# Performance work log

Hardware: AMD Instinct MI355X
Metric: run time of the kernel (lower is better)

The kernel has to match this reference:

```python
import jax, jax.numpy as jnp
import numpy as np

B = 256      # graph pairs
NPG = 28     # nodes per graph
MAXN = 32    # max_node_set_size
EPG = 64     # edges per graph (== max_edge_set_size, so no edge padding)
MAXE = 64
D = 128      # node_state_dim
FN = 32      # raw node feature dim
FE = 32      # raw edge feature dim
SK = 64      # sinkhorn_feature_dim
STEPS = 3    # propagation_steps
TEMP = 0.1
ITERS = 20
CW = 0.9     # consistency_weight
G = 2 * B
N = G * NPG
E = G * EPG


def _lin(key, fi, fo):
    return jax.random.normal(key, (fi, fo), jnp.float32) / np.sqrt(fi)


def setup_inputs() -> dict:
    key = jax.random.key(0)
    ks = jax.random.split(key, 12)
    rng = np.random.default_rng(0)
    off = (np.arange(G) * NPG)[:, None]   # graphs ordered q0,c0,q1,c1,...
    from_idx = jnp.asarray((rng.integers(0, NPG, (G, EPG)) + off).reshape(-1), jnp.int32)
    to_idx = jnp.asarray((rng.integers(0, NPG, (G, EPG)) + off).reshape(-1), jnp.int32)
    return dict(
        node_features=jax.random.normal(ks[0], (N, FN), jnp.float32),
        edge_features=jax.random.normal(ks[1], (E, FE), jnp.float32),
        enc_nw=_lin(ks[2], FN, D), enc_nb=jnp.zeros((D,), jnp.float32),
        enc_ew=_lin(ks[3], FE, D), enc_eb=jnp.zeros((D,), jnp.float32),
        msg_w1=_lin(ks[4], 3 * D, 2 * D), msg_b1=jnp.zeros((2 * D,), jnp.float32),
        msg_w2=_lin(ks[5], 2 * D, D), msg_b2=jnp.zeros((D,), jnp.float32),
        rmsg_w1=_lin(ks[6], 3 * D, 2 * D), rmsg_b1=jnp.zeros((2 * D,), jnp.float32),
        rmsg_w2=_lin(ks[7], 2 * D, D), rmsg_b2=jnp.zeros((D,), jnp.float32),
        upd_w1=_lin(ks[8], 2 * D, 2 * D), upd_b1=jnp.zeros((2 * D,), jnp.float32),
        upd_w2=_lin(ks[9], 2 * D, D), upd_b2=jnp.zeros((D,), jnp.float32),
        sk_w1=_lin(ks[10], D, SK), sk_b1=jnp.zeros((SK,), jnp.float32),
        sk_w2=_lin(ks[11], SK, SK), sk_b2=jnp.zeros((SK,), jnp.float32),
        from_idx=from_idx, to_idx=to_idx,
        query_sizes=jnp.full((B,), NPG, jnp.int32),
        corpus_sizes=jnp.full((B,), NPG, jnp.int32),
    )


def _mlp2(x, w1, b1, w2, b2):
    return jnp.maximum(x @ w1 + b1, 0.0) @ w2 + b2


def _sinkhorn(log_alpha):
    # log-domain sinkhorn (noise_factor = 0 -> deterministic)
    la = log_alpha / TEMP
    for _ in range(ITERS):
        la = la - jax.nn.logsumexp(la, axis=2, keepdims=True)
        la = la - jax.nn.logsumexp(la, axis=1, keepdims=True)
    return jnp.exp(la)


def _align(q, c, plan):
    # feature_alignment_score: -relu(q - P @ c).sum over set and feature dims
    return -jnp.maximum(q - plan @ c, 0.0).sum(axis=(1, 2))


def _forward(node_features, edge_features, enc_nw, enc_nb, enc_ew, enc_eb,
             msg_w1, msg_b1, msg_w2, msg_b2, rmsg_w1, rmsg_b1, rmsg_w2, rmsg_b2,
             upd_w1, upd_b1, upd_w2, upd_b2, sk_w1, sk_b1, sk_w2, sk_b2,
             from_idx, to_idx, query_sizes, corpus_sizes):
    h = node_features @ enc_nw + enc_nb        # encoder, [N, D]
    e = edge_features @ enc_ew + enc_eb        # [E, D]

    def messages(h):
        f = _mlp2(jnp.concatenate([h[from_idx], h[to_idx], e], -1), msg_w1, msg_b1, msg_w2, msg_b2)
        r = _mlp2(jnp.concatenate([h[to_idx], h[from_idx], e], -1), rmsg_w1, rmsg_b1, rmsg_w2, rmsg_b2)
        return f, r

    for _ in range(STEPS):  # GraphPropLayer x propagation_steps
        f, r = messages(h)
        agg = jax.ops.segment_sum(f, to_idx, num_segments=N) + \
              jax.ops.segment_sum(r, from_idx, num_segments=N)
        h = h + _mlp2(jnp.concatenate([agg, h], -1), upd_w1, upd_b1, upd_w2, upd_b2)

    # split_and_stack nodes: graphs alternate query/corpus, pad NPG -> MAXN
    hs = jnp.pad(h.reshape(B, 2, NPG, D), ((0, 0), (0, 0), (0, MAXN - NPG), (0, 0)))
    q_nodes, c_nodes = hs[:, 0], hs[:, 1]      # [B, MAXN, D]

    tq = _mlp2(q_nodes, sk_w1, sk_b1, sk_w2, sk_b2)
    tc = _mlp2(c_nodes, sk_w1, sk_b1, sk_w2, sk_b2)
    pos = jnp.arange(MAXN)[None, :]
    mq = tq * (pos < query_sizes[:, None])[..., None]
    mc = tc * (pos < corpus_sizes[:, None])[..., None]
    node_plan = _sinkhorn(jnp.einsum('bqd,bcd->bqc', mq, mc))   # [B, MAXN, MAXN]

    # propagation_messages on final node states
    f, r = messages(h)
    em = (f + r).reshape(B, 2, EPG, D)         # EPG == MAXE -> no pad
    q_edges, c_edges = em[:, 0], em[:, 1]

    # local (within-graph) endpoint indices for kronecker lookup
    fl = (from_idx % NPG).reshape(B, 2, EPG)
    tl = (to_idx % NPG).reshape(B, 2, EPG)
    qf, cf = fl[:, 0], fl[:, 1]
    qt, ct = tl[:, 0], tl[:, 1]

    def kron(T, qf, qt, cf, ct):
        straight = T[qf][:, cf] * T[qt][:, ct]   # [MAXE, MAXE]
        cross = T[qf][:, ct] * T[qt][:, cf]
        return straight + cross

    edge_scores = jax.vmap(kron)(node_plan, qf, qt, cf, ct)     # [B, MAXE, MAXE]
    edge_plan = _sinkhorn(edge_scores)

    return _align(q_nodes, c_nodes, node_plan) + CW * _align(q_edges, c_edges, edge_plan)


def reference(node_features, edge_features, enc_nw, enc_nb, enc_ew, enc_eb,
              msg_w1, msg_b1, msg_w2, msg_b2, rmsg_w1, rmsg_b1, rmsg_w2, rmsg_b2,
              upd_w1, upd_b1, upd_w2, upd_b2, sk_w1, sk_b1, sk_w2, sk_b2,
              from_idx, to_idx, query_sizes, corpus_sizes):
    return _forward(node_features, edge_features, enc_nw, enc_nb, enc_ew, enc_eb,
                    msg_w1, msg_b1, msg_w2, msg_b2, rmsg_w1, rmsg_b1, rmsg_w2, rmsg_b2,
                    upd_w1, upd_b1, upd_w2, upd_b2, sk_w1, sk_b1, sk_w2, sk_b2,
                    from_idx, to_idx, query_sizes, corpus_sizes)
```

## Files before the change

kernel.cpp:

```cpp
#include <hip/hip_runtime.h>
#include <math.h>

#define NPG 28
#define EPG 64
#define NB  256
#define NG  512
#define NN  14336
#define NE  32768
#define TEMPINV 10.0f
#define SINK_ITERS 20
#define CW 0.9f

typedef unsigned int uint;
typedef unsigned short ushort;
typedef __attribute__((ext_vector_type(8))) __bf16 bf16x8;
typedef __attribute__((ext_vector_type(4))) float f32x4;

__device__ __forceinline__ ushort f2bf(float x) {
    uint u = __float_as_uint(x);
    u += 0x7fffu + ((u >> 16) & 1u);
    return (ushort)(u >> 16);
}
__device__ __forceinline__ uint f2bf2(float lo, float hi) {
    return (uint)f2bf(lo) | ((uint)f2bf(hi) << 16);
}
__device__ __forceinline__ float bflo(uint w) { return __uint_as_float(w << 16); }
__device__ __forceinline__ float bfhi(uint w) { return __uint_as_float(w & 0xffff0000u); }
__device__ __forceinline__ uint relu_sum_pk(uint w1, uint w2, uint w3) {
    float lo = fmaxf(bflo(w1) + bflo(w2) + bflo(w3), 0.f);
    float hi = fmaxf(bfhi(w1) + bfhi(w2) + bfhi(w3), 0.f);
    return f2bf2(lo, hi);
}
__device__ __forceinline__ f32x4 mfma16(bf16x8 a, bf16x8 b, f32x4 c) {
    return __builtin_amdgcn_mfma_f32_16x16x32_bf16(a, b, c, 0, 0, 0);
}

__global__ __launch_bounds__(512, 4) void gnn_fused(
    float* __restrict__ h,
    const ushort* __restrict__ EC2,
    const ushort* __restrict__ WhpL,
    const ushort* __restrict__ W2fL, const ushort* __restrict__ W2rL,
    const float* __restrict__ b2f, const float* __restrict__ b2r,
    const ushort* __restrict__ UW1T, const float* __restrict__ ub1,
    const ushort* __restrict__ UW2T, const float* __restrict__ ub2,
    const int* __restrict__ from_idx, const int* __restrict__ to_idx,
    float* __restrict__ EM)
{
    __shared__ ushort HPs[NPG * 520];
    __shared__ float acc_s[NPG * 132];
    __shared__ float hs[NPG * 132];
    __shared__ int fl[64], tl[64];
    const int g = blockIdx.x;
    const int tid = threadIdx.x;
    const int w = tid >> 6, lane = tid & 63;
    const int li = lane & 15, quad = lane >> 4;
    const int wm = w >> 1, wn = w & 1;
    ushort* hid = &HPs[0];

    if (tid < 64) {
        fl[tid] = from_idx[g * 64 + tid] - g * NPG;
        tl[tid] = to_idx[g * 64 + tid] - g * NPG;
    }
    for (int u = tid; u < NPG * 128; u += 512)
        hs[(u >> 7) * 132 + (u & 127)] = h[(size_t)g * (NPG * 128) + u];
    __syncthreads();

#pragma unroll 1
    for (int step = 0; step < 3; ++step) {
        uint4 ha[2][4];
#pragma unroll
        for (int mi = 0; mi < 2; ++mi) {
            const int row = mi * 16 + li;
            const int rr = (row < NPG) ? row : 0;
#pragma unroll
            for (int kb = 0; kb < 4; ++kb) {
                const float* src = &hs[rr * 132 + kb * 32 + quad * 8];
                const float4 f0 = *(const float4*)src;
                const float4 f1 = *(const float4*)(src + 4);
                uint4 o;
                o.x = f2bf2(f0.x, f0.y);
                o.y = f2bf2(f0.z, f0.w);
                o.z = f2bf2(f1.x, f1.y);
                o.w = f2bf2(f1.z, f1.w);
                ha[mi][kb] = o;
            }
        }
        for (int u = tid; u < NPG * 132; u += 512) acc_s[u] = 0.f;

        f32x4 acc[4];
#pragma unroll
        for (int j = 0; j < 4; ++j) acc[j] = f32x4{0.f, 0.f, 0.f, 0.f};

#pragma unroll 1
        for (int p = 0; p < 2; ++p) {
            {
                const int colw = w * 64;
#pragma unroll
                for (int ni = 0; ni < 4; ++ni) {
                    const int col = colw + ni * 16 + li;
                    const ushort* pb = WhpL + (size_t)(p * 512 + col) * 32 + quad * 8;
                    f32x4 c0 = f32x4{0.f, 0.f, 0.f, 0.f};
                    f32x4 c1 = f32x4{0.f, 0.f, 0.f, 0.f};
#pragma unroll
                    for (int kb = 0; kb < 4; ++kb) {
                        const bf16x8 b = __builtin_bit_cast(bf16x8,
                            *(const uint4*)(pb + (size_t)kb * 32768));
                        c0 = mfma16(__builtin_bit_cast(bf16x8, ha[0][kb]), b, c0);
                        c1 = mfma16(__builtin_bit_cast(bf16x8, ha[1][kb]), b, c1);
                    }
#pragma unroll
                    for (int r = 0; r < 4; ++r) {
                        const int r0 = quad * 4 + r;
                        HPs[r0 * 520 + col] = f2bf(c0[r]);
                        const int r1 = 16 + quad * 4 + r;
                        if (r1 < NPG) HPs[r1 * 520 + col] = f2bf(c1[r]);
                    }
                }
            }
            __syncthreads();
            if (p == 1) {
#pragma unroll
                for (int j = 0; j < 4; ++j) acc[j] = f32x4{0.f, 0.f, 0.f, 0.f};
            }
            const int e = wm * 16 + li;
            const int i1 = p ? tl[e] : fl[e];
            const int i2 = p ? fl[e] : tl[e];
            const int ad1 = i1 * 520 + quad * 8;
            const int ad2 = i2 * 520 + 256 + quad * 8;
            const int ade = e * 32 + quad * 8;
            const ushort* ecb = EC2 + (size_t)(g * 2 + p) * 16384;
            const ushort* W2L = p ? W2rL : W2fL;
            const int n0 = wn * 64;
            const ushort* pb[4];
#pragma unroll
            for (int ni = 0; ni < 4; ++ni)
                pb[ni] = W2L + (size_t)(n0 + ni * 16 + li) * 32 + quad * 8;
#pragma unroll
            for (int kb = 0; kb < 8; ++kb) {
                const uint4 u1 = *(const uint4*)&HPs[ad1 + kb * 32];
                const uint4 u2 = *(const uint4*)&HPs[ad2 + kb * 32];
                const uint4 ue = *(const uint4*)(ecb + kb * 2048 + ade);
                uint4 o;
                o.x = relu_sum_pk(u1.x, u2.x, ue.x);
                o.y = relu_sum_pk(u1.y, u2.y, ue.y);
                o.z = relu_sum_pk(u1.z, u2.z, ue.z);
                o.w = relu_sum_pk(u1.w, u2.w, ue.w);
                const bf16x8 a = __builtin_bit_cast(bf16x8, o);
#pragma unroll
                for (int ni = 0; ni < 4; ++ni) {
                    const bf16x8 b = __builtin_bit_cast(bf16x8,
                        *(const uint4*)(pb[ni] + (size_t)kb * 4096));
                    acc[ni] = mfma16(a, b, acc[ni]);
                }
            }
            {
                const int* targ = p ? fl : tl;
                const float* bias = p ? b2r : b2f;
                float bv[4];
#pragma unroll
                for (int ni = 0; ni < 4; ++ni) bv[ni] = bias[n0 + ni * 16 + li];
#pragma unroll
                for (int r = 0; r < 4; ++r) {
                    const int loc = targ[wm * 16 + quad * 4 + r];
#pragma unroll
                    for (int ni = 0; ni < 4; ++ni)
                        atomicAdd(&acc_s[loc * 132 + n0 + ni * 16 + li],
                                  acc[ni][r] + bv[ni]);
                }
            }
            __syncthreads();
        }

        {
            const int n0u = w * 32;
            f32x4 ua[2][2];
#pragma unroll
            for (int mi = 0; mi < 2; ++mi)
#pragma unroll
                for (int ni = 0; ni < 2; ++ni) ua[mi][ni] = f32x4{0.f, 0.f, 0.f, 0.f};
            const ushort* pb0 = UW1T + (size_t)(n0u + li) * 256 + quad * 8;
            const ushort* pb1 = UW1T + (size_t)(n0u + 16 + li) * 256 + quad * 8;
#pragma unroll
            for (int kb = 0; kb < 8; ++kb) {
                bf16x8 a[2];
                if (kb < 4) {
#pragma unroll
                    for (int mi = 0; mi < 2; ++mi) {
                        const int row = mi * 16 + li;
                        const int rr = (row < NPG) ? row : 0;
                        const float* src = &acc_s[rr * 132 + kb * 32 + quad * 8];
                        const float4 f0 = *(const float4*)src;
                        const float4 f1 = *(const float4*)(src + 4);
                        uint4 o;
                        o.x = f2bf2(f0.x, f0.y);
                        o.y = f2bf2(f0.z, f0.w);
                        o.z = f2bf2(f1.x, f1.y);
                        o.w = f2bf2(f1.z, f1.w);
                        a[mi] = __builtin_bit_cast(bf16x8, o);
                    }
                } else {
                    a[0] = __builtin_bit_cast(bf16x8, ha[0][kb - 4]);
                    a[1] = __builtin_bit_cast(bf16x8, ha[1][kb - 4]);
                }
                const bf16x8 b0 = __builtin_bit_cast(bf16x8, *(const uint4*)(pb0 + kb * 32));
                const bf16x8 b1 = __builtin_bit_cast(bf16x8, *(const uint4*)(pb1 + kb * 32));
#pragma unroll
                for (int mi = 0; mi < 2; ++mi) {
                    ua[mi][0] = mfma16(a[mi], b0, ua[mi][0]);
                    ua[mi][1] = mfma16(a[mi], b1, ua[mi][1]);
                }
            }
            const float bv0 = ub1[n0u + li], bv1 = ub1[n0u + 16 + li];
#pragma unroll
            for (int mi = 0; mi < 2; ++mi)
#pragma unroll
                for (int r = 0; r < 4; ++r) {
                    const int row = mi * 16 + quad * 4 + r;
                    if (row < NPG) {
                        hid[row * 264 + n0u + li] = f2bf(fmaxf(ua[mi][0][r] + bv0, 0.f));
                        hid[row * 264 + n0u + 16 + li] = f2bf(fmaxf(ua[mi][1][r] + bv1, 0.f));
                    }
                }
        }
        __syncthreads();
        {
            const int n0u = w * 16;
            f32x4 ua[2];
            ua[0] = f32x4{0.f, 0.f, 0.f, 0.f};
            ua[1] = f32x4{0.f, 0.f, 0.f, 0.f};
            const ushort* pb0 = UW2T + (size_t)(n0u + li) * 256 + quad * 8;
#pragma unroll
            for (int kb = 0; kb < 8; ++kb) {
                bf16x8 a[2];
#pragma unroll
                for (int mi = 0; mi < 2; ++mi) {
                    const int row = mi * 16 + li;
                    const int rr = (row < NPG) ? row : 0;
                    a[mi] = __builtin_bit_cast(bf16x8,
                        *(const uint4*)&hid[rr * 264 + kb * 32 + quad * 8]);
                }
                const bf16x8 b0 = __builtin_bit_cast(bf16x8, *(const uint4*)(pb0 + kb * 32));
                ua[0] = mfma16(a[0], b0, ua[0]);
                ua[1] = mfma16(a[1], b0, ua[1]);
            }
            const float bv = ub2[n0u + li];
#pragma unroll
            for (int mi = 0; mi < 2; ++mi)
#pragma unroll
                for (int r = 0; r < 4; ++r) {
                    const int row = mi * 16 + quad * 4 + r;
                    if (row < NPG)
                        hs[row * 132 + n0u + li] += ua[mi][r] + bv;
                }
        }
        __syncthreads();
    }

    {
        uint4 ha[2][4];
#pragma unroll
        for (int mi = 0; mi < 2; ++mi) {
            const int row = mi * 16 + li;
            const int rr = (row < NPG) ? row : 0;
#pragma unroll
            for (int kb = 0; kb < 4; ++kb) {
                const float* src = &hs[rr * 132 + kb * 32 + quad * 8];
                const float4 f0 = *(const float4*)src;
                const float4 f1 = *(const float4*)(src + 4);
                uint4 o;
                o.x = f2bf2(f0.x, f0.y);
                o.y = f2bf2(f0.z, f0.w);
                o.z = f2bf2(f1.x, f1.y);
                o.w = f2bf2(f1.z, f1.w);
                ha[mi][kb] = o;
            }
        }
        f32x4 acc[4];
#pragma unroll
        for (int j = 0; j < 4; ++j) acc[j] = f32x4{0.f, 0.f, 0.f, 0.f};
        const int n0 = wn * 64;
#pragma unroll 1
        for (int p = 0; p < 2; ++p) {
            {
                const int colw = w * 64;
#pragma unroll
                for (int ni = 0; ni < 4; ++ni) {
                    const int col = colw + ni * 16 + li;
                    const ushort* pb = WhpL + (size_t)(p * 512 + col) * 32 + quad * 8;
                    f32x4 c0 = f32x4{0.f, 0.f, 0.f, 0.f};
                    f32x4 c1 = f32x4{0.f, 0.f, 0.f, 0.f};
#pragma unroll
                    for (int kb = 0; kb < 4; ++kb) {
                        const bf16x8 b = __builtin_bit_cast(bf16x8,
                            *(const uint4*)(pb + (size_t)kb * 32768));
                        c0 = mfma16(__builtin_bit_cast(bf16x8, ha[0][kb]), b, c0);
                        c1 = mfma16(__builtin_bit_cast(bf16x8, ha[1][kb]), b, c1);
                    }
#pragma unroll
                    for (int r = 0; r < 4; ++r) {
                        const int r0 = quad * 4 + r;
                        HPs[r0 * 520 + col] = f2bf(c0[r]);
                        const int r1 = 16 + quad * 4 + r;
                        if (r1 < NPG) HPs[r1 * 520 + col] = f2bf(c1[r]);
                    }
                }
            }
            __syncthreads();
            const int e = wm * 16 + li;
            const int i1 = p ? tl[e] : fl[e];
            const int i2 = p ? fl[e] : tl[e];
            const int ad1 = i1 * 520 + quad * 8;
            const int ad2 = i2 * 520 + 256 + quad * 8;
            const int ade = e * 32 + quad * 8;
            const ushort* ecb = EC2 + (size_t)(g * 2 + p) * 16384;
            const ushort* W2L = p ? W2rL : W2fL;
            const ushort* pb[4];
#pragma unroll
            for (int ni = 0; ni < 4; ++ni)
                pb[ni] = W2L + (size_t)(n0 + ni * 16 + li) * 32 + quad * 8;
#pragma unroll
            for (int kb = 0; kb < 8; ++kb) {
                const uint4 u1 = *(const uint4*)&HPs[ad1 + kb * 32];
                const uint4 u2 = *(const uint4*)&HPs[ad2 + kb * 32];
                const uint4 ue = *(const uint4*)(ecb + kb * 2048 + ade);
                uint4 o;
                o.x = relu_sum_pk(u1.x, u2.x, ue.x);
                o.y = relu_sum_pk(u1.y, u2.y, ue.y);
                o.z = relu_sum_pk(u1.z, u2.z, ue.z);
                o.w = relu_sum_pk(u1.w, u2.w, ue.w);
                const bf16x8 a = __builtin_bit_cast(bf16x8, o);
#pragma unroll
                for (int ni = 0; ni < 4; ++ni) {
                    const bf16x8 b = __builtin_bit_cast(bf16x8,
                        *(const uint4*)(pb[ni] + (size_t)kb * 4096));
                    acc[ni] = mfma16(a, b, acc[ni]);
                }
            }
            __syncthreads();
        }
        float bv[4];
#pragma unroll
        for (int ni = 0; ni < 4; ++ni)
            bv[ni] = b2f[n0 + ni * 16 + li] + b2r[n0 + ni * 16 + li];
#pragma unroll
        for (int r = 0; r < 4; ++r) {
            const int erow = g * 64 + wm * 16 + quad * 4 + r;
#pragma unroll
            for (int ni = 0; ni < 4; ++ni)
                EM[(size_t)erow * 128 + n0 + ni * 16 + li] = acc[ni][r] + bv[ni];
        }
    }
    for (int u = tid; u < NPG * 128; u += 512)
        h[(size_t)g * (NPG * 128) + u] = hs[(u >> 7) * 132 + (u & 127)];
}

template<int TM, bool OUTBF, bool OUT2, bool ECL>
__global__ __launch_bounds__(256) void gemm2(
    const float* __restrict__ A, int lda, int K,
    const float* __restrict__ W, int ldw, const float* __restrict__ bias,
    float* __restrict__ C, ushort* __restrict__ Cb, int ldc)
{
    constexpr int BM = TM * 16;
    constexpr int AV = BM / 64;
    __shared__ float As[16][BM + 4];
    __shared__ float Bs[16][132];
    const int tid = threadIdx.x;
    const int m0 = blockIdx.x * BM;
    const int n0 = blockIdx.y * 128;
    const int tx = tid & 15, ty = tid >> 4;
    const int arow = (AV == 2) ? (tid >> 1) : (tid >> 2);
    const int a0   = (AV == 2) ? ((tid & 1) * 8) : ((tid & 3) * 4);
    const int brow = ty;
    const int bcol = tx * 8;
    const int nch = K >> 4;

    float4 aC[2], bC[2], aN[2], bN[2];
    float acc[TM][8];
#pragma unroll
    for (int i = 0; i < TM; ++i)
#pragma unroll
        for (int j = 0; j < 8; ++j) acc[i][j] = 0.f;

    {
        const float* src = A + (size_t)(m0 + arow) * lda + a0;
        aC[0] = *(const float4*)src;
        if (AV == 2) aC[1] = *(const float4*)(src + 4);
        const float* bsrc = W + (size_t)brow * ldw + n0 + bcol;
        bC[0] = *(const float4*)bsrc;
        bC[1] = *(const float4*)(bsrc + 4);
    }

    for (int ch = 0; ch < nch; ++ch) {
        {
            const float* f = (const float*)aC;
#pragma unroll
            for (int i = 0; i < AV * 4; ++i) As[a0 + i][arow] = f[i];
            *(float4*)&Bs[brow][bcol]     = bC[0];
            *(float4*)&Bs[brow][bcol + 4] = bC[1];
        }
        __syncthreads();
        if (ch + 1 < nch) {
            const int kc = (ch + 1) << 4;
            const float* src = A + (size_t)(m0 + arow) * lda + kc + a0;
            aN[0] = *(const float4*)src;
            if (AV == 2) aN[1] = *(const float4*)(src + 4);
            const float* bsrc = W + (size_t)(kc + brow) * ldw + n0 + bcol;
            bN[0] = *(const float4*)bsrc;
            bN[1] = *(const float4*)(bsrc + 4);
        }
#pragma unroll
        for (int kk = 0; kk < 16; ++kk) {
            float afr[TM], bfr[8];
#pragma unroll
            for (int i = 0; i < TM; i += 4)
                *(float4*)&afr[i] = *(const float4*)&As[kk][ty * TM + i];
            *(float4*)&bfr[0] = *(const float4*)&Bs[kk][tx * 8];
            *(float4*)&bfr[4] = *(const float4*)&Bs[kk][tx * 8 + 4];
#pragma unroll
            for (int i = 0; i < TM; ++i)
#pragma unroll
                for (int j = 0; j < 8; ++j) acc[i][j] = fmaf(afr[i], bfr[j], acc[i][j]);
        }
        __syncthreads();
        aC[0] = aN[0]; aC[1] = aN[1];
        bC[0] = bN[0]; bC[1] = bN[1];
    }
#pragma unroll
    for (int i = 0; i < TM; ++i) {
        const int row = m0 + ty * TM + i;
#pragma unroll
        for (int j = 0; j < 8; ++j) {
            const int col = n0 + tx * 8 + j;
            float v = acc[i][j] + bias[col];
            if (ECL) {
                const int gg = row >> 6, eloc = row & 63;
                const int p = col >> 8, kb = (col >> 5) & 7, jj = col & 31;
                Cb[(size_t)(((gg * 2 + p) * 8 + kb)) * 2048 + eloc * 32 + jj] = f2bf(v);
            } else if (OUTBF) {
                Cb[(size_t)row * ldc + col] = f2bf(v);
            } else {
                C[(size_t)row * ldc + col] = v;
                if (OUT2) Cb[(size_t)row * ldc + col] = f2bf(v);
            }
        }
    }
}

__global__ __launch_bounds__(256) void pack2(
    const float* __restrict__ msg_w1, const float* __restrict__ rmsg_w1,
    const float* __restrict__ msg_b1, const float* __restrict__ rmsg_b1,
    const float* __restrict__ enc_ew, const float* __restrict__ enc_eb,
    const float* __restrict__ msg_w2, const float* __restrict__ rmsg_w2,
    const float* __restrict__ upd_w1, const float* __restrict__ upd_w2,
    float* __restrict__ Wcomb, float* __restrict__ bcomb,
    ushort* __restrict__ WhpL, ushort* __restrict__ W2fL, ushort* __restrict__ W2rL,
    ushort* __restrict__ UW1T, ushort* __restrict__ UW2T)
{
    const int gid = blockIdx.x, tid = threadIdx.x;
    if (gid < 64) {
        const int idx = gid * 256 + tid;
        const int a = idx >> 9, n = idx & 511;
        const float* Wsrc = (n < 256) ? msg_w1 : rmsg_w1;
        const int nc = n & 255;
        float s = 0.f;
        for (int j = 0; j < 128; ++j)
            s = fmaf(enc_ew[a * 128 + j], Wsrc[(256 + j) * 256 + nc], s);
        Wcomb[idx] = s;
    } else if (gid < 66) {
        const int n = (gid - 64) * 256 + tid;
        const float* Wsrc = (n < 256) ? msg_w1 : rmsg_w1;
        const float* bsrc = (n < 256) ? msg_b1 : rmsg_b1;
        const int nc = n & 255;
        float s = bsrc[nc];
        for (int j = 0; j < 128; ++j)
            s = fmaf(enc_eb[j], Wsrc[(256 + j) * 256 + nc], s);
        bcomb[n] = s;
    } else if (gid < 578) {
        const int idx = (gid - 66) * 256 + tid;
        const int n = idx >> 7, k = idx & 127;
        const float* Wsrc = (n < 512) ? msg_w1 : rmsg_w1;
        const int part = (n >> 8) & 1, col = n & 255;
        WhpL[(size_t)(k >> 5) * 32768 + n * 32 + (k & 31)] =
            f2bf(Wsrc[(part * 128 + k) * 256 + col]);
    } else if (gid < 706) {
        const int idx = (gid - 578) * 256 + tid;
        const int n = idx >> 8, k = idx & 255;
        W2fL[(size_t)(k >> 5) * 4096 + n * 32 + (k & 31)] = f2bf(msg_w2[k * 128 + n]);
    } else if (gid < 834) {
        const int idx = (gid - 706) * 256 + tid;
        const int n = idx >> 8, k = idx & 255;
        W2rL[(size_t)(k >> 5) * 4096 + n * 32 + (k & 31)] = f2bf(rmsg_w2[k * 128 + n]);
    } else if (gid < 1090) {
        const int idx = (gid - 834) * 256 + tid;
        const int n = idx >> 8, k = idx & 255;
        UW1T[idx] = f2bf(upd_w1[k * 256 + n]);
    } else {
        const int idx = (gid - 1090) * 256 + tid;
        const int n = idx >> 8, k = idx & 255;
        UW2T[idx] = f2bf(upd_w2[k * 128 + n]);
    }
}

__global__ __launch_bounds__(256) void node_kernel(
    const float* __restrict__ h,
    const float* __restrict__ w1, const float* __restrict__ b1,
    const float* __restrict__ w2, const float* __restrict__ b2,
    const int* __restrict__ qsz, const int* __restrict__ csz,
    float* __restrict__ plan_out, float* __restrict__ loss_out)
{
    __shared__ float qn[32][128];
    __shared__ float cn[32][128];
    __shared__ float t1[32][64];
    __shared__ float mq[32][68];
    __shared__ float mc[32][68];
    __shared__ float la[32][33];
    __shared__ float red[4];
    const int bb = blockIdx.x;
    const int tid = threadIdx.x;
    const int qs = qsz[bb], cs = csz[bb];
    for (int u = tid * 4; u < 4096; u += 1024) {
        const int p = u >> 7, d = u & 127;
        float4 zq = make_float4(0.f, 0.f, 0.f, 0.f), zc = zq;
        if (p < NPG) {
            zq = *(const float4*)(h + (size_t)((2 * bb) * NPG + p) * 128 + d);
            zc = *(const float4*)(h + (size_t)((2 * bb + 1) * NPG + p) * 128 + d);
        }
        *(float4*)&qn[p][d] = zq;
        *(float4*)&cn[p][d] = zc;
    }
    __syncthreads();
    const int col = tid & 63;
    const int rg  = tid >> 6;
    for (int s = 0; s < 2; ++s) {
        const float (*src)[128] = s ? cn : qn;
        float (*dst)[68] = s ? mc : mq;
        const int sz = s ? cs : qs;
        float a8[8];
#pragma unroll
        for (int u = 0; u < 8; ++u) a8[u] = b1[col];
        for (int k = 0; k < 128; ++k) {
            const float wv = w1[k * 64 + col];
#pragma unroll
            for (int u = 0; u < 8; ++u) a8[u] = fmaf(src[rg + 4 * u][k], wv, a8[u]);
        }
#pragma unroll
        for (int u = 0; u < 8; ++u) t1[rg + 4 * u][col] = fmaxf(a8[u], 0.f);
        __syncthreads();
#pragma unroll
        for (int u = 0; u < 8; ++u) a8[u] = b2[col];
        for (int k = 0; k < 64; ++k) {
            const float wv = w2[k * 64 + col];
#pragma unroll
            for (int u = 0; u < 8; ++u) a8[u] = fmaf(t1[rg + 4 * u][k], wv, a8[u]);
        }
#pragma unroll
        for (int u = 0; u < 8; ++u) {
            const int r = rg + 4 * u;
            dst[r][col] = (r < sz) ? a8[u] : 0.f;
        }
        __syncthreads();
    }
    {
        const int q = tid >> 3, cg = tid & 7;
#pragma unroll
        for (int u = 0; u < 4; ++u) {
            const int c = cg + 8 * u;
            float s = 0.f;
            for (int d = 0; d < 64; ++d) s = fmaf(mq[q][d], mc[c][d], s);
            la[q][c] = s * TEMPINV;
        }
    }
    __syncthreads();
    const int l8 = tid & 7, rq = tid >> 3;
    for (int it = 0; it < SINK_ITERS; ++it) {
        {
            float x[4];
#pragma unroll
            for (int u = 0; u < 4; ++u) x[u] = la[rq][l8 * 4 + u];
            float m = fmaxf(fmaxf(x[0], x[1]), fmaxf(x[2], x[3]));
            m = fmaxf(m, __shfl_xor(m, 1));
            m = fmaxf(m, __shfl_xor(m, 2));
            m = fmaxf(m, __shfl_xor(m, 4));
            float s = __expf(x[0] - m) + __expf(x[1] - m) + __expf(x[2] - m) + __expf(x[3] - m);
            s += __shfl_xor(s, 1);
            s += __shfl_xor(s, 2);
            s += __shfl_xor(s, 4);
            const float lse = m + __logf(s);
#pragma unroll
            for (int u = 0; u < 4; ++u) la[rq][l8 * 4 + u] = x[u] - lse;
        }
        __syncthreads();
        {
            float x[4];
#pragma unroll
            for (int u = 0; u < 4; ++u) x[u] = la[l8 * 4 + u][rq];
            float m = fmaxf(fmaxf(x[0], x[1]), fmaxf(x[2], x[3]));
            m = fmaxf(m, __shfl_xor(m, 1));
            m = fmaxf(m, __shfl_xor(m, 2));
            m = fmaxf(m, __shfl_xor(m, 4));
            float s = __expf(x[0] - m) + __expf(x[1] - m) + __expf(x[2] - m) + __expf(x[3] - m);
            s += __shfl_xor(s, 1);
            s += __shfl_xor(s, 2);
            s += __shfl_xor(s, 4);
            const float lse = m + __logf(s);
#pragma unroll
            for (int u = 0; u < 4; ++u) la[l8 * 4 + u][rq] = x[u] - lse;
        }
        __syncthreads();
    }
    for (int u = tid; u < 1024; u += 256) {
        const int q = u >> 5, c = u & 31;
        const float p = __expf(la[q][c]);
        la[q][c] = p;
        plan_out[(size_t)bb * 1024 + u] = p;
    }
    __syncthreads();
    float lsum = 0.f;
    {
        const int q = tid >> 3, dg = tid & 7;
        for (int u = 0; u < 16; ++u) {
            const int d = dg + 8 * u;
            float pc = 0.f;
#pragma unroll
            for (int c = 0; c < 32; ++c) pc = fmaf(la[q][c], cn[c][d], pc);
            lsum += fmaxf(qn[q][d] - pc, 0.f);
        }
    }
#pragma unroll
    for (int off = 1; off < 64; off <<= 1) lsum += __shfl_xor(lsum, off);
    if ((tid & 63) == 0) red[tid >> 6] = lsum;
    __syncthreads();
    if (tid == 0) loss_out[bb] = -(red[0] + red[1] + red[2] + red[3]);
}

__global__ __launch_bounds__(256) void edge_kernel(
    const float* __restrict__ plan, const float* __restrict__ EM,
    const int* __restrict__ from_idx, const int* __restrict__ to_idx,
    float* __restrict__ loss_out)
{
    __shared__ float T[32][33];
    __shared__ float la[64][65];
    __shared__ float ce[64][128];
    __shared__ int qf[64], qt[64], cfi[64], cti[64];
    __shared__ float red[4];
    const int bb = blockIdx.x;
    const int tid = threadIdx.x;
    for (int u = tid; u < 1024; u += 256) T[u >> 5][u & 31] = plan[(size_t)bb * 1024 + u];
    if (tid < 64) {
        const int gq = 2 * bb, gc = 2 * bb + 1;
        qf[tid]  = from_idx[gq * 64 + tid] - gq * NPG;
        qt[tid]  = to_idx  [gq * 64 + tid] - gq * NPG;
        cfi[tid] = from_idx[gc * 64 + tid] - gc * NPG;
        cti[tid] = to_idx  [gc * 64 + tid] - gc * NPG;
    }
    {
        const int gc = 2 * bb + 1;
        for (int u = tid * 4; u < 8192; u += 1024) {
            const int i = u >> 7, d = u & 127;
            *(float4*)&ce[i][d] = *(const float4*)(EM + (size_t)(gc * 64 + i) * 128 + d);
        }
    }
    __syncthreads();
    {
        const int i = tid >> 2, jg = tid & 3;
        const int a = qf[i], b_ = qt[i];
#pragma unroll
        for (int u = 0; u < 16; ++u) {
            const int j = jg * 16 + u;
            const float s = T[a][cfi[j]] * T[b_][cti[j]] + T[a][cti[j]] * T[b_][cfi[j]];
            la[i][j] = s * TEMPINV;
        }
    }
    __syncthreads();
    const int l4 = tid & 3, rr = tid >> 2;
    for (int it = 0; it < SINK_ITERS; ++it) {
        {
            float x[16];
#pragma unroll
            for (int u = 0; u < 16; ++u) x[u] = la[rr][l4 * 16 + u];
            float m = x[0];
#pragma unroll
            for (int u = 1; u < 16; ++u) m = fmaxf(m, x[u]);
            m = fmaxf(m, __shfl_xor(m, 1));
            m = fmaxf(m, __shfl_xor(m, 2));
            float s = 0.f;
#pragma unroll
            for (int u = 0; u < 16; ++u) s += __expf(x[u] - m);
            s += __shfl_xor(s, 1);
            s += __shfl_xor(s, 2);
            const float lse = m + __logf(s);
#pragma unroll
            for (int u = 0; u < 16; ++u) la[rr][l4 * 16 + u] = x[u] - lse;
        }
        __syncthreads();
        {
            float x[16];
#pragma unroll
            for (int u = 0; u < 16; ++u) x[u] = la[l4 * 16 + u][rr];
            float m = x[0];
#pragma unroll
            for (int u = 1; u < 16; ++u) m = fmaxf(m, x[u]);
            m = fmaxf(m, __shfl_xor(m, 1));
            m = fmaxf(m, __shfl_xor(m, 2));
            float s = 0.f;
#pragma unroll
            for (int u = 0; u < 16; ++u) s += __expf(x[u] - m);
            s += __shfl_xor(s, 1);
            s += __shfl_xor(s, 2);
            const float lse = m + __logf(s);
#pragma unroll
            for (int u = 0; u < 16; ++u) la[l4 * 16 + u][rr] = x[u] - lse;
        }
        __syncthreads();
    }
    for (int u = tid; u < 4096; u += 256) la[u >> 6][u & 63] = __expf(la[u >> 6][u & 63]);
    __syncthreads();
    float lsum = 0.f;
    {
        const int q = tid >> 2, dg = tid & 3;
        const float* qe = EM + (size_t)((2 * bb) * 64 + q) * 128;
        for (int u = 0; u < 32; ++u) {
            const int d = dg + 4 * u;
            float pc = 0.f;
            for (int c = 0; c < 64; ++c) pc = fmaf(la[q][c], ce[c][d], pc);
            lsum += fmaxf(qe[d] - pc, 0.f);
        }
    }
#pragma unroll
    for (int off = 1; off < 64; off <<= 1) lsum += __shfl_xor(lsum, off);
    if ((tid & 63) == 0) red[tid >> 6] = lsum;
    __syncthreads();
    if (tid == 0) loss_out[bb] -= CW * (red[0] + red[1] + red[2] + red[3]);
}

extern "C" void kernel_launch(void* const* d_in, const int* in_sizes, int n_in,
                              void* d_out, int out_size, void* d_ws, size_t ws_size,
                              hipStream_t stream)
{
    const float* node_features = (const float*)d_in[0];
    const float* edge_features = (const float*)d_in[1];
    const float* enc_nw  = (const float*)d_in[2];
    const float* enc_nb  = (const float*)d_in[3];
    const float* enc_ew  = (const float*)d_in[4];
    const float* enc_eb  = (const float*)d_in[5];
    const float* msg_w1  = (const float*)d_in[6];
    const float* msg_b1  = (const float*)d_in[7];
    const float* msg_w2  = (const float*)d_in[8];
    const float* msg_b2  = (const float*)d_in[9];
    const float* rmsg_w1 = (const float*)d_in[10];
    const float* rmsg_b1 = (const float*)d_in[11];
    const float* rmsg_w2 = (const float*)d_in[12];
    const float* rmsg_b2 = (const float*)d_in[13];
    const float* upd_w1  = (const float*)d_in[14];
    const float* upd_b1  = (const float*)d_in[15];
    const float* upd_w2  = (const float*)d_in[16];
    const float* upd_b2  = (const float*)d_in[17];
    const float* sk_w1   = (const float*)d_in[18];
    const float* sk_b1   = (const float*)d_in[19];
    const float* sk_w2   = (const float*)d_in[20];
    const float* sk_b2   = (const float*)d_in[21];
    const int* from_idx  = (const int*)d_in[22];
    const int* to_idx    = (const int*)d_in[23];
    const int* qsizes    = (const int*)d_in[24];
    const int* csizes    = (const int*)d_in[25];
    float* out = (float*)d_out;

    float* ws    = (float*)d_ws;
    float* h     = ws;
    float* EM    = h + (size_t)NN * 128;
    float* plan  = EM + (size_t)NE * 128;
    float* Wcomb = plan + (size_t)NB * 1024;
    float* bcomb = Wcomb + 16384;
    ushort* EC2  = (ushort*)(bcomb + 512);
    ushort* WhpL = EC2 + (size_t)NE * 512;
    ushort* W2fL = WhpL + 131072;
    ushort* W2rL = W2fL + 32768;
    ushort* UW1T = W2rL + 32768;
    ushort* UW2T = UW1T + 65536;

    const dim3 blk(256);
    const dim3 blk512(512);

    pack2<<<1218, blk, 0, stream>>>(msg_w1, rmsg_w1, msg_b1, rmsg_b1,
                                    enc_ew, enc_eb, msg_w2, rmsg_w2, upd_w1, upd_w2,
                                    Wcomb, bcomb, WhpL, W2fL, W2rL, UW1T, UW2T);
    gemm2<4, false, false, false><<<dim3(NN / 64, 1), blk, 0, stream>>>(
        node_features, 32, 32, enc_nw, 128, enc_nb, h, nullptr, 128);
    gemm2<8, false, false, true><<<dim3(NE / 128, 4), blk, 0, stream>>>(
        edge_features, 32, 32, Wcomb, 512, bcomb, nullptr, EC2, 512);

    gnn_fused<<<dim3(NG), blk512, 0, stream>>>(
        h, EC2, WhpL, W2fL, W2rL, msg_b2, rmsg_b2,
        UW1T, upd_b1, UW2T, upd_b2, from_idx, to_idx, EM);

    node_kernel<<<NB, blk, 0, stream>>>(
        h, sk_w1, sk_b1, sk_w2, sk_b2, qsizes, csizes, plan, out);
    edge_kernel<<<NB, blk, 0, stream>>>(
        plan, EM, from_idx, to_idx, out);
}
```

Measured before the change: 553.7 us.

## Fuse node and edge encoder GEMMs into gnn_fused with LDS-resident edge contributions

Removes the two separate fp32 encoder GEMM launches and computes the node encoding and the combined edge-encoder/message-W1 projection inside gnn_fused with bf16 MFMA. The per-graph edge contribution is stored in a new 64 KB LDS buffer instead of a global EC2 array, so it is no longer written to and re-read from global memory. Weights are pre-packed to bf16 in pack2. The cost is much higher LDS use per block, and the launch-bounds occupancy hint is dropped. The node encoder now runs in bf16 rather than fp32.

```diff
diff --git a/kernel.cpp b/kernel.cpp
--- a/kernel.cpp
+++ b/kernel.cpp
@@ -31,22 +31,34 @@
     float hi = fmaxf(bfhi(w1) + bfhi(w2) + bfhi(w3), 0.f);
     return f2bf2(lo, hi);
 }
+__device__ __forceinline__ uint4 pack_f32x8(const float* src) {
+    const float4 f0 = *(const float4*)src;
+    const float4 f1 = *(const float4*)(src + 4);
+    uint4 o;
+    o.x = f2bf2(f0.x, f0.y);
+    o.y = f2bf2(f0.z, f0.w);
+    o.z = f2bf2(f1.x, f1.y);
+    o.w = f2bf2(f1.z, f1.w);
+    return o;
+}
 __device__ __forceinline__ f32x4 mfma16(bf16x8 a, bf16x8 b, f32x4 c) {
     return __builtin_amdgcn_mfma_f32_16x16x32_bf16(a, b, c, 0, 0, 0);
 }
 
-__global__ __launch_bounds__(512, 4) void gnn_fused(
-    float* __restrict__ h,
-    const ushort* __restrict__ EC2,
+__global__ __launch_bounds__(512) void gnn_fused(
+    const float* __restrict__ nf, const float* __restrict__ ef,
+    const ushort* __restrict__ encL, const float* __restrict__ enc_nb,
+    const ushort* __restrict__ WcombL, const float* __restrict__ bcomb,
     const ushort* __restrict__ WhpL,
     const ushort* __restrict__ W2fL, const ushort* __restrict__ W2rL,
     const float* __restrict__ b2f, const float* __restrict__ b2r,
     const ushort* __restrict__ UW1T, const float* __restrict__ ub1,
     const ushort* __restrict__ UW2T, const float* __restrict__ ub2,
     const int* __restrict__ from_idx, const int* __restrict__ to_idx,
-    float* __restrict__ EM)
+    float* __restrict__ h, float* __restrict__ EM)
 {
     __shared__ ushort HPs[NPG * 520];
+    __shared__ ushort ECs[2 * 8 * 2048];
     __shared__ float acc_s[NPG * 132];
     __shared__ float hs[NPG * 132];
     __shared__ int fl[64], tl[64];
@@ -61,8 +73,65 @@
         fl[tid] = from_idx[g * 64 + tid] - g * NPG;
         tl[tid] = to_idx[g * 64 + tid] - g * NPG;
     }
-    for (int u = tid; u < NPG * 128; u += 512)
-        hs[(u >> 7) * 132 + (u & 127)] = h[(size_t)g * (NPG * 128) + u];
+
+    {
+        uint4 anf[2];
+#pragma unroll
+        for (int mi = 0; mi < 2; ++mi) {
+            const int row = mi * 16 + li;
+            const int rr = (row < NPG) ? row : 0;
+            const float4 f0 = *(const float4*)(nf + ((size_t)g * NPG + rr) * 32 + quad * 8);
+            const float4 f1 = *(const float4*)(nf + ((size_t)g * NPG + rr) * 32 + quad * 8 + 4);
+            uint4 o;
+            o.x = f2bf2(f0.x, f0.y); o.y = f2bf2(f0.z, f0.w);
+            o.z = f2bf2(f1.x, f1.y); o.w = f2bf2(f1.z, f1.w);
+            anf[mi] = o;
+        }
+        const int col = w * 16 + li;
+        const bf16x8 b = __builtin_bit_cast(bf16x8,
+            *(const uint4*)(encL + (size_t)col * 32 + quad * 8));
+        f32x4 c0 = mfma16(__builtin_bit_cast(bf16x8, anf[0]), b, f32x4{0.f, 0.f, 0.f, 0.f});
+        f32x4 c1 = mfma16(__builtin_bit_cast(bf16x8, anf[1]), b, f32x4{0.f, 0.f, 0.f, 0.f});
+        const float bv = enc_nb[col];
+#pragma unroll
+        for (int r = 0; r < 4; ++r) {
+            const int r0 = quad * 4 + r;
+            hs[r0 * 132 + col] = c0[r] + bv;
+            const int r1 = 16 + quad * 4 + r;
+            if (r1 < NPG) hs[r1 * 132 + col] = c1[r] + bv;
+        }
+    }
+    {
+        uint4 aef[4];
+#pragma unroll
+        for (int mi = 0; mi < 4; ++mi) {
+            const int e = mi * 16 + li;
+            const float4 f0 = *(const float4*)(ef + ((size_t)g * 64 + e) * 32 + quad * 8);
+            const float4 f1 = *(const float4*)(ef + ((size_t)g * 64 + e) * 32 + quad * 8 + 4);
+            uint4 o;
+            o.x = f2bf2(f0.x, f0.y); o.y = f2bf2(f0.z, f0.w);
+            o.z = f2bf2(f1.x, f1.y); o.w = f2bf2(f1.z, f1.w);
+            aef[mi] = o;
+        }
+#pragma unroll
+        for (int ni = 0; ni < 4; ++ni) {
+            const int col = w * 64 + ni * 16 + li;
+            const bf16x8 b = __builtin_bit_cast(bf16x8,
+                *(const uint4*)(WcombL + (size_t)col * 32 + quad * 8));
+            const float bv = bcomb[col];
+            const int pp = col >> 8, kbl = (col >> 5) & 7, j = col & 31;
+#pragma unroll
+            for (int mi = 0; mi < 4; ++mi) {
+                f32x4 c = mfma16(__builtin_bit_cast(bf16x8, aef[mi]), b,
+                                 f32x4{0.f, 0.f, 0.f, 0.f});
+#pragma unroll
+                for (int r = 0; r < 4; ++r) {
+                    const int e = mi * 16 + quad * 4 + r;
+                    ECs[pp * 16384 + kbl * 2048 + e * 32 + j] = f2bf(c[r] + bv);
+                }
+            }
+        }
+    }
     __syncthreads();
 
 #pragma unroll 1
@@ -73,17 +142,8 @@
             const int row = mi * 16 + li;
             const int rr = (row < NPG) ? row : 0;
 #pragma unroll
-            for (int kb = 0; kb < 4; ++kb) {
-                const float* src = &hs[rr * 132 + kb * 32 + quad * 8];
-                const float4 f0 = *(const float4*)src;
-                const float4 f1 = *(const float4*)(src + 4);
-                uint4 o;
-                o.x = f2bf2(f0.x, f0.y);
-                o.y = f2bf2(f0.z, f0.w);
-                o.z = f2bf2(f1.x, f1.y);
-                o.w = f2bf2(f1.z, f1.w);
-                ha[mi][kb] = o;
-            }
+            for (int kb = 0; kb < 4; ++kb)
+                ha[mi][kb] = pack_f32x8(&hs[rr * 132 + kb * 32 + quad * 8]);
         }
         for (int u = tid; u < NPG * 132; u += 512) acc_s[u] = 0.f;
 
@@ -118,6 +178,7 @@
                 }
             }
             __syncthreads();
+
             if (p == 1) {
 #pragma unroll
                 for (int j = 0; j < 4; ++j) acc[j] = f32x4{0.f, 0.f, 0.f, 0.f};
@@ -127,8 +188,7 @@
             const int i2 = p ? fl[e] : tl[e];
             const int ad1 = i1 * 520 + quad * 8;
             const int ad2 = i2 * 520 + 256 + quad * 8;
-            const int ade = e * 32 + quad * 8;
-            const ushort* ecb = EC2 + (size_t)(g * 2 + p) * 16384;
+            const int ade = p * 16384 + e * 32 + quad * 8;
             const ushort* W2L = p ? W2rL : W2fL;
             const int n0 = wn * 64;
             const ushort* pb[4];
@@ -139,7 +199,7 @@
             for (int kb = 0; kb < 8; ++kb) {
                 const uint4 u1 = *(const uint4*)&HPs[ad1 + kb * 32];
                 const uint4 u2 = *(const uint4*)&HPs[ad2 + kb * 32];
-                const uint4 ue = *(const uint4*)(ecb + kb * 2048 + ade);
+                const uint4 ue = *(const uint4*)&ECs[ade + kb * 2048];
                 uint4 o;
                 o.x = relu_sum_pk(u1.x, u2.x, ue.x);
                 o.y = relu_sum_pk(u1.y, u2.y, ue.y);
@@ -188,15 +248,8 @@
                     for (int mi = 0; mi < 2; ++mi) {
                         const int row = mi * 16 + li;
                         const int rr = (row < NPG) ? row : 0;
-                        const float* src = &acc_s[rr * 132 + kb * 32 + quad * 8];
-                        const float4 f0 = *(const float4*)src;
-                        const float4 f1 = *(const float4*)(src + 4);
-                        uint4 o;
-                        o.x = f2bf2(f0.x, f0.y);
-                        o.y = f2bf2(f0.z, f0.w);
-                        o.z = f2bf2(f1.x, f1.y);
-                        o.w = f2bf2(f1.z, f1.w);
-                        a[mi] = __builtin_bit_cast(bf16x8, o);
+                        a[mi] = __builtin_bit_cast(bf16x8,
+                            pack_f32x8(&acc_s[rr * 132 + kb * 32 + quad * 8]));
                     }
                 } else {
                     a[0] = __builtin_bit_cast(bf16x8, ha[0][kb - 4]);
@@ -263,17 +316,8 @@
             const int row = mi * 16 + li;
             const int rr = (row < NPG) ? row : 0;
 #pragma unroll
-            for (int kb = 0; kb < 4; ++kb) {
-                const float* src = &hs[rr * 132 + kb * 32 + quad * 8];
-                const float4 f0 = *(const float4*)src;
-                const float4 f1 = *(const float4*)(src + 4);
-                uint4 o;
-                o.x = f2bf2(f0.x, f0.y);
-                o.y = f2bf2(f0.z, f0.w);
-                o.z = f2bf2(f1.x, f1.y);
-                o.w = f2bf2(f1.z, f1.w);
-                ha[mi][kb] = o;
-            }
+            for (int kb = 0; kb < 4; ++kb)
+                ha[mi][kb] = pack_f32x8(&hs[rr * 132 + kb * 32 + quad * 8]);
         }
         f32x4 acc[4];
 #pragma unroll
@@ -311,8 +355,7 @@
             const int i2 = p ? fl[e] : tl[e];
             const int ad1 = i1 * 520 + quad * 8;
             const int ad2 = i2 * 520 + 256 + quad * 8;
-            const int ade = e * 32 + quad * 8;
-            const ushort* ecb = EC2 + (size_t)(g * 2 + p) * 16384;
+            const int ade = p * 16384 + e * 32 + quad * 8;
             const ushort* W2L = p ? W2rL : W2fL;
             const ushort* pb[4];
 #pragma unroll
@@ -322,7 +365,7 @@
             for (int kb = 0; kb < 8; ++kb) {
                 const uint4 u1 = *(const uint4*)&HPs[ad1 + kb * 32];
                 const uint4 u2 = *(const uint4*)&HPs[ad2 + kb * 32];
-                const uint4 ue = *(const uint4*)(ecb + kb * 2048 + ade);
+                const uint4 ue = *(const uint4*)&ECs[ade + kb * 2048];
                 uint4 o;
                 o.x = relu_sum_pk(u1.x, u2.x, ue.x);
                 o.y = relu_sum_pk(u1.y, u2.y, ue.y);
@@ -354,105 +397,15 @@
         h[(size_t)g * (NPG * 128) + u] = hs[(u >> 7) * 132 + (u & 127)];
 }
 
-template<int TM, bool OUTBF, bool OUT2, bool ECL>
-__global__ __launch_bounds__(256) void gemm2(
-    const float* __restrict__ A, int lda, int K,
-    const float* __restrict__ W, int ldw, const float* __restrict__ bias,
-    float* __restrict__ C, ushort* __restrict__ Cb, int ldc)
-{
-    constexpr int BM = TM * 16;
-    constexpr int AV = BM / 64;
-    __shared__ float As[16][BM + 4];
-    __shared__ float Bs[16][132];
-    const int tid = threadIdx.x;
-    const int m0 = blockIdx.x * BM;
-    const int n0 = blockIdx.y * 128;
-    const int tx = tid & 15, ty = tid >> 4;
-    const int arow = (AV == 2) ? (tid >> 1) : (tid >> 2);
-    const int a0   = (AV == 2) ? ((tid & 1) * 8) : ((tid & 3) * 4);
-    const int brow = ty;
-    const int bcol = tx * 8;
-    const int nch = K >> 4;
-
-    float4 aC[2], bC[2], aN[2], bN[2];
-    float acc[TM][8];
-#pragma unroll
-    for (int i = 0; i < TM; ++i)
-#pragma unroll
-        for (int j = 0; j < 8; ++j) acc[i][j] = 0.f;
-
-    {
-        const float* src = A + (size_t)(m0 + arow) * lda + a0;
-        aC[0] = *(const float4*)src;
-        if (AV == 2) aC[1] = *(const float4*)(src + 4);
-        const float* bsrc = W + (size_t)brow * ldw + n0 + bcol;
-        bC[0] = *(const float4*)bsrc;
-        bC[1] = *(const float4*)(bsrc + 4);
-    }
-
-    for (int ch = 0; ch < nch; ++ch) {
-        {
-            const float* f = (const float*)aC;
-#pragma unroll
-            for (int i = 0; i < AV * 4; ++i) As[a0 + i][arow] = f[i];
-            *(float4*)&Bs[brow][bcol]     = bC[0];
-            *(float4*)&Bs[brow][bcol + 4] = bC[1];
-        }
-        __syncthreads();
-        if (ch + 1 < nch) {
-            const int kc = (ch + 1) << 4;
-            const float* src = A + (size_t)(m0 + arow) * lda + kc + a0;
-            aN[0] = *(const float4*)src;
-            if (AV == 2) aN[1] = *(const float4*)(src + 4);
-            const float* bsrc = W + (size_t)(kc + brow) * ldw + n0 + bcol;
-            bN[0] = *(const float4*)bsrc;
-            bN[1] = *(const float4*)(bsrc + 4);
-        }
-#pragma unroll
-        for (int kk = 0; kk < 16; ++kk) {
-            float afr[TM], bfr[8];
-#pragma unroll
-            for (int i = 0; i < TM; i += 4)
-                *(float4*)&afr[i] = *(const float4*)&As[kk][ty * TM + i];
-            *(float4*)&bfr[0] = *(const float4*)&Bs[kk][tx * 8];
-            *(float4*)&bfr[4] = *(const float4*)&Bs[kk][tx * 8 + 4];
-#pragma unroll
-            for (int i = 0; i < TM; ++i)
-#pragma unroll
-                for (int j = 0; j < 8; ++j) acc[i][j] = fmaf(afr[i], bfr[j], acc[i][j]);
-        }
-        __syncthreads();
-        aC[0] = aN[0]; aC[1] = aN[1];
-        bC[0] = bN[0]; bC[1] = bN[1];
-    }
-#pragma unroll
-    for (int i = 0; i < TM; ++i) {
-        const int row = m0 + ty * TM + i;
-#pragma unroll
-        for (int j = 0; j < 8; ++j) {
-            const int col = n0 + tx * 8 + j;
-            float v = acc[i][j] + bias[col];
-            if (ECL) {
-                const int gg = row >> 6, eloc = row & 63;
-                const int p = col >> 8, kb = (col >> 5) & 7, jj = col & 31;
-                Cb[(size_t)(((gg * 2 + p) * 8 + kb)) * 2048 + eloc * 32 + jj] = f2bf(v);
-            } else if (OUTBF) {
-                Cb[(size_t)row * ldc + col] = f2bf(v);
-            } else {
-                C[(size_t)row * ldc + col] = v;
-                if (OUT2) Cb[(size_t)row * ldc + col] = f2bf(v);
-            }
-        }
-    }
-}
-
 __global__ __launch_bounds__(256) void pack2(
     const float* __restrict__ msg_w1, const float* __restrict__ rmsg_w1,
     const float* __restrict__ msg_b1, const float* __restrict__ rmsg_b1,
     const float* __restrict__ enc_ew, const float* __restrict__ enc_eb,
+    const float* __restrict__ enc_nw,
     const float* __restrict__ msg_w2, const float* __restrict__ rmsg_w2,
     const float* __restrict__ upd_w1, const float* __restrict__ upd_w2,
-    float* __restrict__ Wcomb, float* __restrict__ bcomb,
+    ushort* __restrict__ WcombL, float* __restrict__ bcomb,
+    ushort* __restrict__ encL,
     ushort* __restrict__ WhpL, ushort* __restrict__ W2fL, ushort* __restrict__ W2rL,
     ushort* __restrict__ UW1T, ushort* __restrict__ UW2T)
 {
@@ -465,7 +418,7 @@
         float s = 0.f;
         for (int j = 0; j < 128; ++j)
             s = fmaf(enc_ew[a * 128 + j], Wsrc[(256 + j) * 256 + nc], s);
-        Wcomb[idx] = s;
+        WcombL[n * 32 + a] = f2bf(s);
     } else if (gid < 66) {
         const int n = (gid - 64) * 256 + tid;
         const float* Wsrc = (n < 256) ? msg_w1 : rmsg_w1;
@@ -475,27 +428,31 @@
         for (int j = 0; j < 128; ++j)
             s = fmaf(enc_eb[j], Wsrc[(256 + j) * 256 + nc], s);
         bcomb[n] = s;
-    } else if (gid < 578) {
+    } else if (gid < 82) {
         const int idx = (gid - 66) * 256 + tid;
+        const int n = idx >> 5, k = idx & 31;
+        encL[idx] = f2bf(enc_nw[k * 128 + n]);
+    } else if (gid < 594) {
+        const int idx = (gid - 82) * 256 + tid;
         const int n = idx >> 7, k = idx & 127;
         const float* Wsrc = (n < 512) ? msg_w1 : rmsg_w1;
         const int part = (n >> 8) & 1, col = n & 255;
         WhpL[(size_t)(k >> 5) * 32768 + n * 32 + (k & 31)] =
             f2bf(Wsrc[(part * 128 + k) * 256 + col]);
-    } else if (gid < 706) {
-        const int idx = (gid - 578) * 256 + tid;
+    } else if (gid < 722) {
+        const int idx = (gid - 594) * 256 + tid;
         const int n = idx >> 8, k = idx & 255;
         W2fL[(size_t)(k >> 5) * 4096 + n * 32 + (k & 31)] = f2bf(msg_w2[k * 128 + n]);
-    } else if (gid < 834) {
-        const int idx = (gid - 706) * 256 + tid;
+    } else if (gid < 850) {
+        const int idx = (gid - 722) * 256 + tid;
         const int n = idx >> 8, k = idx & 255;
         W2rL[(size_t)(k >> 5) * 4096 + n * 32 + (k & 31)] = f2bf(rmsg_w2[k * 128 + n]);
-    } else if (gid < 1090) {
-        const int idx = (gid - 834) * 256 + tid;
+    } else if (gid < 1106) {
+        const int idx = (gid - 850) * 256 + tid;
         const int n = idx >> 8, k = idx & 255;
         UW1T[idx] = f2bf(upd_w1[k * 256 + n]);
     } else {
-        const int idx = (gid - 1090) * 256 + tid;
+        const int idx = (gid - 1106) * 256 + tid;
         const int n = idx >> 8, k = idx & 255;
         UW2T[idx] = f2bf(upd_w2[k * 128 + n]);
     }
@@ -765,33 +722,31 @@
     const int* csizes    = (const int*)d_in[25];
     float* out = (float*)d_out;
 
-    float* ws    = (float*)d_ws;
-    float* h     = ws;
-    float* EM    = h + (size_t)NN * 128;
-    float* plan  = EM + (size_t)NE * 128;
-    float* Wcomb = plan + (size_t)NB * 1024;
-    float* bcomb = Wcomb + 16384;
-    ushort* EC2  = (ushort*)(bcomb + 512);
-    ushort* WhpL = EC2 + (size_t)NE * 512;
-    ushort* W2fL = WhpL + 131072;
-    ushort* W2rL = W2fL + 32768;
-    ushort* UW1T = W2rL + 32768;
-    ushort* UW2T = UW1T + 65536;
+    float* ws     = (float*)d_ws;
+    float* h      = ws;
+    float* EM     = h + (size_t)NN * 128;
+    float* plan   = EM + (size_t)NE * 128;
+    float* bcomb  = plan + (size_t)NB * 1024;
+    ushort* WcombL = (ushort*)(bcomb + 512);
+    ushort* encL  = WcombL + 16384;
+    ushort* WhpL  = encL + 4096;
+    ushort* W2fL  = WhpL + 131072;
+    ushort* W2rL  = W2fL + 32768;
+    ushort* UW1T  = W2rL + 32768;
+    ushort* UW2T  = UW1T + 65536;
 
     const dim3 blk(256);
     const dim3 blk512(512);
 
-    pack2<<<1218, blk, 0, stream>>>(msg_w1, rmsg_w1, msg_b1, rmsg_b1,
-                                    enc_ew, enc_eb, msg_w2, rmsg_w2, upd_w1, upd_w2,
-                                    Wcomb, bcomb, WhpL, W2fL, W2rL, UW1T, UW2T);
-    gemm2<4, false, false, false><<<dim3(NN / 64, 1), blk, 0, stream>>>(
-        node_features, 32, 32, enc_nw, 128, enc_nb, h, nullptr, 128);
-    gemm2<8, false, false, true><<<dim3(NE / 128, 4), blk, 0, stream>>>(
-        edge_features, 32, 32, Wcomb, 512, bcomb, nullptr, EC2, 512);
+    pack2<<<1234, blk, 0, stream>>>(msg_w1, rmsg_w1, msg_b1, rmsg_b1,
+                                    enc_ew, enc_eb, enc_nw, msg_w2, rmsg_w2,
+                                    upd_w1, upd_w2,
+                                    WcombL, bcomb, encL, WhpL, W2fL, W2rL, UW1T, UW2T);
 
     gnn_fused<<<dim3(NG), blk512, 0, stream>>>(
-        h, EC2, WhpL, W2fL, W2rL, msg_b2, rmsg_b2,
-        UW1T, upd_b1, UW2T, upd_b2, from_idx, to_idx, EM);
+        node_features, edge_features, encL, enc_nb, WcombL, bcomb,
+        WhpL, W2fL, W2rL, msg_b2, rmsg_b2,
+        UW1T, upd_b1, UW2T, upd_b2, from_idx, to_idx, h, EM);
 
     node_kernel<<<NB, blk, 0, stream>>>(
         h, sk_w1, sk_b1, sk_w2, sk_b2, qsizes, csizes, plan, out);
```

Result: faster. 468.9 us, median of 2 (-15.3%).
